# Optimization experiments

Measured on AMD Instinct MI355X. Metric: run time of the kernel, lower is better.

Reference implementation:

```python
import jax, jax.numpy as jnp
import numpy as np
import math

C = 128

def setup_inputs() -> dict:
    key = jax.random.key(0)
    ks = jax.random.split(key, 6)
    B, N, M = 4, 8192, 2048
    s = 1.0 / math.sqrt(C)
    return {
        "pcd_up": jax.random.normal(ks[0], (B, C, N), dtype=jnp.float32),
        "pcd_down": jax.random.normal(ks[1], (B, C, M), dtype=jnp.float32),
        "wq": jax.random.normal(ks[2], (C, C), dtype=jnp.float32) * s,
        "wk": jax.random.normal(ks[3], (C, C), dtype=jnp.float32) * s,
        "wv": jax.random.normal(ks[4], (C, C), dtype=jnp.float32) * s,
        "wskip": jax.random.normal(ks[5], (C, C), dtype=jnp.float32) * s,
    }

def reference(pcd_up, pcd_down, wq, wk, wv, wskip):
    # Conv1d(kernel=1, no bias) == per-point linear: w @ x over channel dim
    q = jnp.einsum('oc,bcn->bon', wq, pcd_up)      # [B,C,N]
    k = jnp.einsum('oc,bcm->bom', wk, pcd_down)    # [B,C,M]
    v = jnp.einsum('oc,bcm->bom', wv, pcd_down)    # [B,C,M]
    energy = jnp.einsum('bcn,bcm->bnm', q, k)      # [B,N,M]
    scale = math.sqrt(q.shape[1])                  # sqrt(C): q.shape[-2] in torch
    attn = jax.nn.softmax(energy / scale, axis=-1)
    x = jnp.einsum('bnm,bcm->bcn', attn, v)        # [B,C,N]
    skip = jnp.einsum('oc,bcn->bon', wskip, pcd_up)
    return skip + x
```

## Files before the change

kernel.cpp:

```cpp
#include <hip/hip_runtime.h>
#include <hip/hip_bf16.h>
#include <math.h>

#define C_DIM 128
#define B_DIM 4
#define N_DIM 8192
#define M_DIM 2048
#define NT_KV 32

typedef unsigned short u16;
typedef unsigned int u32;
typedef short bf16x8 __attribute__((ext_vector_type(8)));
typedef float f32x4 __attribute__((ext_vector_type(4)));
typedef float f32x16 __attribute__((ext_vector_type(16)));
typedef u32 u32x4 __attribute__((ext_vector_type(4)));

__device__ inline u16 f2bf(float f) {
  u32 u = __builtin_bit_cast(u32, f);
  u += 0x7fffu + ((u >> 16) & 1u);
  return (u16)(u >> 16);
}
__device__ inline u32 cvtpk_bf16(float lo, float hi) {
  u32 r;
  asm("v_cvt_pk_bf16_f32 %0, %1, %2" : "=v"(r) : "v"(lo), "v"(hi));
  return r;
}

template <int MODE>
__device__ inline void proj_pass(const float* __restrict__ W, float wscale,
                                 const u16* __restrict__ xt_s,
                                 u16* __restrict__ outh,
                                 int b, int X, int x0, int t) {
  const int l = t & 63, w = t >> 6, lr = l & 15, lh = (l >> 4) & 3;
  bf16x8 wf[2][4];
  #pragma unroll
  for (int ot = 0; ot < 2; ++ot)
    #pragma unroll
    for (int kc = 0; kc < 4; ++kc) {
      const float* wp = &W[(size_t)(w * 32 + ot * 16 + lr) * 128 + kc * 32 + lh * 8];
      float4 a0 = *(const float4*)wp;
      float4 a1 = *(const float4*)(wp + 4);
      bf16x8 f;
      f[0] = (short)f2bf(a0.x * wscale); f[1] = (short)f2bf(a0.y * wscale);
      f[2] = (short)f2bf(a0.z * wscale); f[3] = (short)f2bf(a0.w * wscale);
      f[4] = (short)f2bf(a1.x * wscale); f[5] = (short)f2bf(a1.y * wscale);
      f[6] = (short)f2bf(a1.z * wscale); f[7] = (short)f2bf(a1.w * wscale);
      wf[ot][kc] = f;
    }
  f32x4 acc[2][4];
  #pragma unroll
  for (int ot = 0; ot < 2; ++ot)
    #pragma unroll
    for (int xt = 0; xt < 4; ++xt) acc[ot][xt] = 0.f;

  #pragma unroll
  for (int xt = 0; xt < 4; ++xt) {
    int xx = xt * 16 + lr;
    #pragma unroll
    for (int kc = 0; kc < 4; ++kc) {
      bf16x8 bf = *(const bf16x8*)&xt_s[xx * 128 + ((kc * 32 + lh * 8) ^ ((xx & 15) << 3))];
      #pragma unroll
      for (int ot = 0; ot < 2; ++ot)
        acc[ot][xt] = __builtin_amdgcn_mfma_f32_16x16x32_bf16(wf[ot][kc], bf, acc[ot][xt], 0, 0, 0);
    }
  }
  #pragma unroll
  for (int ot = 0; ot < 2; ++ot) {
    int o0 = w * 32 + ot * 16 + lh * 4;
    #pragma unroll
    for (int xt = 0; xt < 4; ++xt) {
      int xg = x0 + xt * 16 + lr;
      if constexpr (MODE == 0) {
        u16 h[4];
        #pragma unroll
        for (int r = 0; r < 4; ++r) h[r] = f2bf(acc[ot][xt][r]);
        *(uint2*)&outh[((size_t)b * X + xg) * 128 + o0] = *(uint2*)h;
      } else if constexpr (MODE == 2) {
        int tt = xg >> 6, mt = (xg >> 5) & 1, ms = xg & 31;
        int kcK = o0 >> 4, lh1p = (o0 >> 3) & 1, e0 = o0 & 7;
        u16 h[4];
        #pragma unroll
        for (int r = 0; r < 4; ++r) h[r] = f2bf(acc[ot][xt][r]);
        size_t off = ((((size_t)(b * NT_KV + tt) * 2 + mt) * 8 + kcK) * 64 + (ms | (lh1p << 5))) * 8 + e0;
        *(uint2*)&outh[off] = *(uint2*)h;
      } else {
        int tt = xg >> 6, sv = (xg >> 4) & 3, lh1m = (xg >> 3) & 1, e = xg & 7;
        int ctv = o0 >> 5;
        #pragma unroll
        for (int r = 0; r < 4; ++r) {
          int cs = (o0 + r) & 31;
          size_t off = ((((size_t)(b * NT_KV + tt) * 4 + ctv) * 4 + sv) * 64 + (cs | (lh1m << 5))) * 8 + e;
          outh[off] = f2bf(acc[ot][xt][r]);
        }
      }
    }
  }
}

template <int MODE_A, int MODE_B>
__global__ __launch_bounds__(256, 2) void proj_kernel(
    const float* __restrict__ in, const float* __restrict__ WA, const float* __restrict__ WB,
    u16* __restrict__ hA, u16* __restrict__ hB, int X, float wscaleA) {
  __shared__ u16 xt_s[64 * 128];
  const int b = blockIdx.y, x0 = blockIdx.x * 64, t = threadIdx.x;
  #pragma unroll
  for (int pp = 0; pp < 8; ++pp) {
    int c = pp * 16 + (t >> 4);
    int x4 = (t & 15) * 4;
    float4 v = *(const float4*)&in[((size_t)b * 128 + c) * X + x0 + x4];
    xt_s[(x4 + 0) * 128 + (c ^ (((x4 + 0) & 15) << 3))] = f2bf(v.x);
    xt_s[(x4 + 1) * 128 + (c ^ (((x4 + 1) & 15) << 3))] = f2bf(v.y);
    xt_s[(x4 + 2) * 128 + (c ^ (((x4 + 2) & 15) << 3))] = f2bf(v.z);
    xt_s[(x4 + 3) * 128 + (c ^ (((x4 + 3) & 15) << 3))] = f2bf(v.w);
  }
  __syncthreads();
  proj_pass<MODE_A>(WA, wscaleA, xt_s, hA, b, X, x0, t);
  if constexpr (MODE_B >= 0)
    proj_pass<MODE_B>(WB, 1.0f, xt_s, hB, b, X, x0, t);
}

__device__ inline void stage_kv(const u16* __restrict__ gK, const u16* __restrict__ gV,
                                u16* lK, u16* lV, int tile, int t) {
  const u16* ks = gK + (size_t)tile * 8192;
  const u16* vs = gV + (size_t)tile * 8192;
  #pragma unroll
  for (int i = 0; i < 4; ++i) {
    int ch = t + i * 256;
    __builtin_amdgcn_global_load_lds((const __attribute__((address_space(1))) void*)(ks + ch * 8),
                                     (__attribute__((address_space(3))) void*)(lK + ch * 8), 16, 0, 0);
    __builtin_amdgcn_global_load_lds((const __attribute__((address_space(1))) void*)(vs + ch * 8),
                                     (__attribute__((address_space(3))) void*)(lV + ch * 8), 16, 0, 0);
  }
}

__global__ __launch_bounds__(256, 2) void attn_kernel(
    const u16* __restrict__ Qt, const u16* __restrict__ Kt2,
    const u16* __restrict__ Vp, const float* __restrict__ up,
    const float* __restrict__ wskip, float* __restrict__ out) {
  __shared__ u16 kv[2][2][8192];

  const int bid = blockIdx.x;
  const int xcd = bid & 7, b = xcd & 3, slot = bid >> 3;
  const int n0 = ((xcd >> 2) * 32 + slot) * 128;
  const int t = threadIdx.x, w = t >> 6, l = t & 63, lh1 = l >> 5;
  const int nq = n0 + w * 32 + (l & 31);

  bf16x8 qf[8];
  #pragma unroll
  for (int kc = 0; kc < 8; ++kc)
    qf[kc] = *(const bf16x8*)&Qt[((size_t)b * N_DIM + nq) * 128 + kc * 16 + lh1 * 8];

  const u16* gK = Kt2 + (size_t)b * 262144;
  const u16* gV = Vp + (size_t)b * 262144;

  f32x16 acco[4];
  #pragma unroll
  for (int ct = 0; ct < 4; ++ct) acco[ct] = 0.f;
  float lrun = 0.f;

  bf16x8 pf[4];
  bf16x8 vreg[16];
  #pragma unroll
  for (int s = 0; s < 4; ++s) pf[s] = (bf16x8)0;
  #pragma unroll
  for (int x = 0; x < 16; ++x) vreg[x] = (bf16x8)0;

  stage_kv(gK, gV, kv[0][0], kv[0][1], 0, t);
  __syncthreads();

  #pragma unroll 2
  for (int i = 0; i < 32; ++i) {
    const int cur = i & 1;
    if (i + 1 < 32)
      stage_kv(gK, gV, kv[cur ^ 1][0], kv[cur ^ 1][1], i + 1, t);
    const u16* kl = kv[cur][0];
    const u16* vl = kv[cur][1];

    f32x16 sacc[2];
    sacc[0] = 0.f; sacc[1] = 0.f;
    __builtin_amdgcn_s_setprio(1);
    #pragma unroll
    for (int kc = 0; kc < 8; ++kc) {
      #pragma unroll
      for (int mt = 0; mt < 2; ++mt) {
        bf16x8 kf = *(const bf16x8*)&kl[((mt * 8 + kc) * 64 + l) * 8];
        sacc[mt] = __builtin_amdgcn_mfma_f32_32x32x16_bf16(kf, qf[kc], sacc[mt], 0, 0, 0);
      }
    }
    #pragma unroll
    for (int s = 0; s < 4; ++s)
      #pragma unroll
      for (int ct = 0; ct < 4; ++ct)
        acco[ct] = __builtin_amdgcn_mfma_f32_32x32x16_bf16(vreg[ct * 4 + s], pf[s], acco[ct], 0, 0, 0);
    __builtin_amdgcn_s_setprio(0);
    __builtin_amdgcn_sched_barrier(0);

    #pragma unroll
    for (int x = 0; x < 16; ++x)
      vreg[x] = *(const bf16x8*)&vl[(x * 64 + l) * 8];

    float rs = 0.f;
    #pragma unroll
    for (int mt = 0; mt < 2; ++mt)
      #pragma unroll
      for (int r = 0; r < 16; ++r) {
        sacc[mt][r] = exp2f(sacc[mt][r]);
        rs += sacc[mt][r];
      }
    lrun += rs;
    u32 gp[8][2];
    #pragma unroll
    for (int mt = 0; mt < 2; ++mt)
      #pragma unroll
      for (int j = 0; j < 4; ++j) {
        gp[mt * 4 + j][0] = cvtpk_bf16(sacc[mt][j * 4 + 0], sacc[mt][j * 4 + 1]);
        gp[mt * 4 + j][1] = cvtpk_bf16(sacc[mt][j * 4 + 2], sacc[mt][j * 4 + 3]);
      }
    #pragma unroll
    for (int s = 0; s < 4; ++s) {
      const int ga = (s >> 1) * 4 + (s & 1) * 2, gb = ga + 1;
      u32 s0 = lh1 ? gp[ga][0] : gp[gb][0];
      u32 s1 = lh1 ? gp[ga][1] : gp[gb][1];
      u32 r0 = (u32)__shfl_xor((int)s0, 32, 64);
      u32 r1 = (u32)__shfl_xor((int)s1, 32, 64);
      u32x4 fv;
      fv.x = lh1 ? r0 : gp[ga][0];
      fv.y = lh1 ? r1 : gp[ga][1];
      fv.z = lh1 ? gp[gb][0] : r0;
      fv.w = lh1 ? gp[gb][1] : r1;
      pf[s] = __builtin_bit_cast(bf16x8, fv);
    }
    __syncthreads();
  }

  __builtin_amdgcn_s_setprio(1);
  #pragma unroll
  for (int s = 0; s < 4; ++s)
    #pragma unroll
    for (int ct = 0; ct < 4; ++ct)
      acco[ct] = __builtin_amdgcn_mfma_f32_32x32x16_bf16(vreg[ct * 4 + s], pf[s], acco[ct], 0, 0, 0);
  __builtin_amdgcn_s_setprio(0);

  float lt = lrun + __shfl_xor(lrun, 32, 64);
  float inv = 1.0f / lt;
  #pragma unroll
  for (int ct = 0; ct < 4; ++ct)
    #pragma unroll
    for (int r = 0; r < 16; ++r) acco[ct][r] *= inv;

  const float* upb = up + (size_t)b * 128 * N_DIM;
  #pragma unroll
  for (int kc = 0; kc < 8; ++kc) {
    float uv[8];
    #pragma unroll
    for (int e = 0; e < 8; ++e)
      uv[e] = upb[(size_t)(kc * 16 + lh1 * 8 + e) * N_DIM + nq];
    u32x4 ufv;
    ufv.x = cvtpk_bf16(uv[0], uv[1]);
    ufv.y = cvtpk_bf16(uv[2], uv[3]);
    ufv.z = cvtpk_bf16(uv[4], uv[5]);
    ufv.w = cvtpk_bf16(uv[6], uv[7]);
    bf16x8 upf = __builtin_bit_cast(bf16x8, ufv);
    #pragma unroll
    for (int ct = 0; ct < 4; ++ct) {
      const float* wp = &wskip[(size_t)(ct * 32 + (l & 31)) * 128 + kc * 16 + lh1 * 8];
      float4 w0 = *(const float4*)wp;
      float4 w1 = *(const float4*)(wp + 4);
      u32x4 wfv;
      wfv.x = cvtpk_bf16(w0.x, w0.y);
      wfv.y = cvtpk_bf16(w0.z, w0.w);
      wfv.z = cvtpk_bf16(w1.x, w1.y);
      wfv.w = cvtpk_bf16(w1.z, w1.w);
      bf16x8 wsf = __builtin_bit_cast(bf16x8, wfv);
      acco[ct] = __builtin_amdgcn_mfma_f32_32x32x16_bf16(wsf, upf, acco[ct], 0, 0, 0);
    }
  }

  #pragma unroll
  for (int ct = 0; ct < 4; ++ct)
    #pragma unroll
    for (int r = 0; r < 16; ++r) {
      int c = ct * 32 + (r & 3) + 8 * (r >> 2) + 4 * lh1;
      out[((size_t)b * 128 + c) * N_DIM + nq] = acco[ct][r];
    }
}

extern "C" void kernel_launch(void* const* d_in, const int* in_sizes, int n_in,
                              void* d_out, int out_size, void* d_ws, size_t ws_size,
                              hipStream_t stream) {
  const float* up    = (const float*)d_in[0];
  const float* down  = (const float*)d_in[1];
  const float* wq    = (const float*)d_in[2];
  const float* wk    = (const float*)d_in[3];
  const float* wv    = (const float*)d_in[4];
  const float* wskip = (const float*)d_in[5];
  float* out = (float*)d_out;

  u16* Qt  = (u16*)d_ws;
  u16* Kt2 = Qt + (size_t)B_DIM * N_DIM * C_DIM;
  u16* Vp  = Kt2 + (size_t)B_DIM * M_DIM * C_DIM;

  const float qscale = (float)(1.4426950408889634 / sqrt(128.0));

  hipLaunchKernelGGL((proj_kernel<0, -1>), dim3(N_DIM / 64, B_DIM), dim3(256), 0, stream,
                     up, wq, nullptr, Qt, nullptr, N_DIM, qscale);
  hipLaunchKernelGGL((proj_kernel<2, 3>), dim3(M_DIM / 64, B_DIM), dim3(256), 0, stream,
                     down, wk, wv, Kt2, Vp, M_DIM, 1.0f);
  hipLaunchKernelGGL((attn_kernel), dim3(256), dim3(256), 0, stream,
                     Qt, Kt2, Vp, up, wskip, out);
}
```

Baseline: 83.16 us.

## Split attention KV range across two blocks with atomic-flag partial merge

Each query tile's KV sweep is split into two halves processed by separate blocks, doubling the grid from 256 to 512 blocks so it better fills the GPU's compute units. Each block writes its unnormalized output and row sums to workspace, and the second block to finish (detected via an atomic counter) adds in the partner's partial and runs the skip/epilogue. This relies on the scores being computed without a running max, so partials can simply be summed. It adds a memset launch, extra global traffic for partials, and fences, and is used only when the workspace is large enough.

Result: slower. 187.3 us (+125.3%).

```diff
diff --git a/kernel.cpp b/kernel.cpp
--- a/kernel.cpp
+++ b/kernel.cpp
@@ -133,17 +133,33 @@
   }
 }
 
+template <int SPLIT>
 __global__ __launch_bounds__(256, 2) void attn_kernel(
     const u16* __restrict__ Qt, const u16* __restrict__ Kt2,
     const u16* __restrict__ Vp, const float* __restrict__ up,
-    const float* __restrict__ wskip, float* __restrict__ out) {
+    const float* __restrict__ wskip, float* __restrict__ out,
+    float* __restrict__ part, float* __restrict__ lpart,
+    unsigned* __restrict__ flags) {
   __shared__ u16 kv[2][2][8192];
+  __shared__ unsigned oldflag_s;
 
   const int bid = blockIdx.x;
   const int xcd = bid & 7, b = xcd & 3, slot = bid >> 3;
-  const int n0 = ((xcd >> 2) * 32 + slot) * 128;
+  int n0, mh, pair;
+  if constexpr (SPLIT == 2) {
+    mh = slot & 1;
+    const int ntile = (xcd >> 2) * 32 + (slot >> 1);
+    n0 = ntile * 128;
+    pair = b * 64 + ntile;
+  } else {
+    mh = 0;
+    n0 = ((xcd >> 2) * 32 + slot) * 128;
+    pair = 0;
+  }
   const int t = threadIdx.x, w = t >> 6, l = t & 63, lh1 = l >> 5;
   const int nq = n0 + w * 32 + (l & 31);
+  const int NT = NT_KV / SPLIT;
+  const int t0 = mh * NT;
 
   bf16x8 qf[8];
   #pragma unroll
@@ -165,14 +181,14 @@
   #pragma unroll
   for (int x = 0; x < 16; ++x) vreg[x] = (bf16x8)0;
 
-  stage_kv(gK, gV, kv[0][0], kv[0][1], 0, t);
+  stage_kv(gK, gV, kv[0][0], kv[0][1], t0, t);
   __syncthreads();
 
   #pragma unroll 2
-  for (int i = 0; i < 32; ++i) {
+  for (int i = 0; i < NT; ++i) {
     const int cur = i & 1;
-    if (i + 1 < 32)
-      stage_kv(gK, gV, kv[cur ^ 1][0], kv[cur ^ 1][1], i + 1, t);
+    if (i + 1 < NT)
+      stage_kv(gK, gV, kv[cur ^ 1][0], kv[cur ^ 1][1], t0 + i + 1, t);
     const u16* kl = kv[cur][0];
     const u16* vl = kv[cur][1];
 
@@ -242,6 +258,30 @@
   __builtin_amdgcn_s_setprio(0);
 
   float lt = lrun + __shfl_xor(lrun, 32, 64);
+
+  if constexpr (SPLIT == 2) {
+    float* myp = part + ((size_t)pair * 2 + mh) * 16384;
+    #pragma unroll
+    for (int ct = 0; ct < 4; ++ct)
+      #pragma unroll
+      for (int r = 0; r < 16; ++r)
+        myp[((w * 4 + ct) * 16 + r) * 64 + l] = acco[ct][r];
+    if (!lh1) lpart[((pair * 2 + mh) * 4 + w) * 32 + (l & 31)] = lt;
+    __threadfence();
+    __syncthreads();
+    if (t == 0) oldflag_s = atomicAdd(&flags[pair], 1u);
+    __syncthreads();
+    if (oldflag_s == 0) return;
+    __threadfence();
+    const float* pp = part + ((size_t)pair * 2 + (mh ^ 1)) * 16384;
+    #pragma unroll
+    for (int ct = 0; ct < 4; ++ct)
+      #pragma unroll
+      for (int r = 0; r < 16; ++r)
+        acco[ct][r] += pp[((w * 4 + ct) * 16 + r) * 64 + l];
+    lt += lpart[((pair * 2 + (mh ^ 1)) * 4 + w) * 32 + (l & 31)];
+  }
+
   float inv = 1.0f / lt;
   #pragma unroll
   for (int ct = 0; ct < 4; ++ct)
@@ -296,9 +336,18 @@
   const float* wskip = (const float*)d_in[5];
   float* out = (float*)d_out;
 
-  u16* Qt  = (u16*)d_ws;
-  u16* Kt2 = Qt + (size_t)B_DIM * N_DIM * C_DIM;
-  u16* Vp  = Kt2 + (size_t)B_DIM * M_DIM * C_DIM;
+  char* ws = (char*)d_ws;
+  u16* Qt  = (u16*)ws;
+  u16* Kt2 = (u16*)(ws + (8u << 20));
+  u16* Vp  = (u16*)(ws + (10u << 20));
+  size_t offPart  = 12u << 20;
+  size_t offLpart = offPart + (size_t)256 * 2 * 16384 * 4;
+  size_t offFlags = offLpart + (size_t)256 * 2 * 128 * 4;
+  size_t need     = offFlags + 256 * sizeof(unsigned);
+  float* part     = (float*)(ws + offPart);
+  float* lpart    = (float*)(ws + offLpart);
+  unsigned* flags = (unsigned*)(ws + offFlags);
+  const bool split = ws_size >= need;
 
   const float qscale = (float)(1.4426950408889634 / sqrt(128.0));
 
@@ -306,6 +355,12 @@
                      up, wq, nullptr, Qt, nullptr, N_DIM, qscale);
   hipLaunchKernelGGL((proj_kernel<2, 3>), dim3(M_DIM / 64, B_DIM), dim3(256), 0, stream,
                      down, wk, wv, Kt2, Vp, M_DIM, 1.0f);
-  hipLaunchKernelGGL((attn_kernel), dim3(256), dim3(256), 0, stream,
-                     Qt, Kt2, Vp, up, wskip, out);
-}
+  if (split) {
+    hipMemsetAsync(flags, 0, 256 * sizeof(unsigned), stream);
+    hipLaunchKernelGGL((attn_kernel<2>), dim3(512), dim3(256), 0, stream,
+                       Qt, Kt2, Vp, up, wskip, out, part, lpart, flags);
+  } else {
+    hipLaunchKernelGGL((attn_kernel<1>), dim3(256), dim3(256), 0, stream,
+                       Qt, Kt2, Vp, up, wskip, out, nullptr, nullptr, nullptr);
+  }
+}
```

## Split each KV tile across two wave groups and reduce partial outputs via LDS

Applied to the files above, without the earlier changes.

Doubles the attention block to 512 threads. Each pair of waves shares the same 32 queries but handles a different half of every 64-key tile, so per-wave MFMA work and register use in the loop are halved and more waves are resident on each CU. Partial output accumulators and row sums from the second wave group are written to shared memory (aliased onto the KV buffers) and summed by the first group, which then does the normalisation and the skip projection. It also replaces the shfl_xor-based P fragment shuffle with v_permlane32_swap. The cost is an extra LDS reduction step with a barrier at the end and half of the waves sitting idle during the epilogue.

Measured after the change: 74.00 us. -11.0%, faster.

```diff
diff --git a/kernel.cpp b/kernel.cpp
--- a/kernel.cpp
+++ b/kernel.cpp
@@ -124,8 +124,8 @@
   const u16* ks = gK + (size_t)tile * 8192;
   const u16* vs = gV + (size_t)tile * 8192;
   #pragma unroll
-  for (int i = 0; i < 4; ++i) {
-    int ch = t + i * 256;
+  for (int i = 0; i < 2; ++i) {
+    int ch = t + i * 512;
     __builtin_amdgcn_global_load_lds((const __attribute__((address_space(1))) void*)(ks + ch * 8),
                                      (__attribute__((address_space(3))) void*)(lK + ch * 8), 16, 0, 0);
     __builtin_amdgcn_global_load_lds((const __attribute__((address_space(1))) void*)(vs + ch * 8),
@@ -133,17 +133,22 @@
   }
 }
 
-__global__ __launch_bounds__(256, 2) void attn_kernel(
+__global__ __launch_bounds__(512, 2) void attn_kernel(
     const u16* __restrict__ Qt, const u16* __restrict__ Kt2,
     const u16* __restrict__ Vp, const float* __restrict__ up,
     const float* __restrict__ wskip, float* __restrict__ out) {
-  __shared__ u16 kv[2][2][8192];
+  __shared__ union {
+    u16 kv[2][2][8192];
+    float od[4][4096];
+  } lds;
+  __shared__ float lb[4][64];
 
   const int bid = blockIdx.x;
   const int xcd = bid & 7, b = xcd & 3, slot = bid >> 3;
   const int n0 = ((xcd >> 2) * 32 + slot) * 128;
   const int t = threadIdx.x, w = t >> 6, l = t & 63, lh1 = l >> 5;
-  const int nq = n0 + w * 32 + (l & 31);
+  const int h = w >> 2;
+  const int nq = n0 + (w & 3) * 32 + (l & 31);
 
   bf16x8 qf[8];
   #pragma unroll
@@ -158,131 +163,141 @@
   for (int ct = 0; ct < 4; ++ct) acco[ct] = 0.f;
   float lrun = 0.f;
 
-  bf16x8 pf[4];
-  bf16x8 vreg[16];
-  #pragma unroll
-  for (int s = 0; s < 4; ++s) pf[s] = (bf16x8)0;
-  #pragma unroll
-  for (int x = 0; x < 16; ++x) vreg[x] = (bf16x8)0;
-
-  stage_kv(gK, gV, kv[0][0], kv[0][1], 0, t);
+  bf16x8 pf[2];
+  bf16x8 vreg[8];
+  #pragma unroll
+  for (int u = 0; u < 2; ++u) pf[u] = (bf16x8)0;
+  #pragma unroll
+  for (int x = 0; x < 8; ++x) vreg[x] = (bf16x8)0;
+
+  stage_kv(gK, gV, lds.kv[0][0], lds.kv[0][1], 0, t);
   __syncthreads();
 
   #pragma unroll 2
-  for (int i = 0; i < 32; ++i) {
+  for (int i = 0; i < NT_KV; ++i) {
     const int cur = i & 1;
-    if (i + 1 < 32)
-      stage_kv(gK, gV, kv[cur ^ 1][0], kv[cur ^ 1][1], i + 1, t);
-    const u16* kl = kv[cur][0];
-    const u16* vl = kv[cur][1];
-
-    f32x16 sacc[2];
-    sacc[0] = 0.f; sacc[1] = 0.f;
+    if (i + 1 < NT_KV)
+      stage_kv(gK, gV, lds.kv[cur ^ 1][0], lds.kv[cur ^ 1][1], i + 1, t);
+    const u16* kl = lds.kv[cur][0];
+    const u16* vl = lds.kv[cur][1];
+
+    f32x16 sacc = 0.f;
     __builtin_amdgcn_s_setprio(1);
     #pragma unroll
     for (int kc = 0; kc < 8; ++kc) {
-      #pragma unroll
-      for (int mt = 0; mt < 2; ++mt) {
-        bf16x8 kf = *(const bf16x8*)&kl[((mt * 8 + kc) * 64 + l) * 8];
-        sacc[mt] = __builtin_amdgcn_mfma_f32_32x32x16_bf16(kf, qf[kc], sacc[mt], 0, 0, 0);
-      }
-    }
-    #pragma unroll
-    for (int s = 0; s < 4; ++s)
+      bf16x8 kf = *(const bf16x8*)&kl[((h * 8 + kc) * 64 + l) * 8];
+      sacc = __builtin_amdgcn_mfma_f32_32x32x16_bf16(kf, qf[kc], sacc, 0, 0, 0);
+    }
+    #pragma unroll
+    for (int u = 0; u < 2; ++u)
       #pragma unroll
       for (int ct = 0; ct < 4; ++ct)
-        acco[ct] = __builtin_amdgcn_mfma_f32_32x32x16_bf16(vreg[ct * 4 + s], pf[s], acco[ct], 0, 0, 0);
+        acco[ct] = __builtin_amdgcn_mfma_f32_32x32x16_bf16(vreg[ct * 2 + u], pf[u], acco[ct], 0, 0, 0);
     __builtin_amdgcn_s_setprio(0);
     __builtin_amdgcn_sched_barrier(0);
 
     #pragma unroll
-    for (int x = 0; x < 16; ++x)
-      vreg[x] = *(const bf16x8*)&vl[(x * 64 + l) * 8];
-
-    float rs = 0.f;
-    #pragma unroll
-    for (int mt = 0; mt < 2; ++mt)
+    for (int ct = 0; ct < 4; ++ct)
+      #pragma unroll
+      for (int u = 0; u < 2; ++u)
+        vreg[ct * 2 + u] = *(const bf16x8*)&vl[((ct * 4 + 2 * h + u) * 64 + l) * 8];
+
+    #pragma unroll
+    for (int r = 0; r < 16; ++r) sacc[r] = exp2f(sacc[r]);
+    {
+      float a0 = (sacc[0] + sacc[1]) + (sacc[2] + sacc[3]);
+      float a1 = (sacc[4] + sacc[5]) + (sacc[6] + sacc[7]);
+      float a2 = (sacc[8] + sacc[9]) + (sacc[10] + sacc[11]);
+      float a3 = (sacc[12] + sacc[13]) + (sacc[14] + sacc[15]);
+      lrun += (a0 + a1) + (a2 + a3);
+    }
+    u32 gp[4][2];
+    #pragma unroll
+    for (int j = 0; j < 4; ++j) {
+      gp[j][0] = cvtpk_bf16(sacc[j * 4 + 0], sacc[j * 4 + 1]);
+      gp[j][1] = cvtpk_bf16(sacc[j * 4 + 2], sacc[j * 4 + 3]);
+    }
+    #pragma unroll
+    for (int u = 0; u < 2; ++u) {
+      u32 a0 = gp[2 * u][0], a1 = gp[2 * u][1];
+      u32 b0 = gp[2 * u + 1][0], b1 = gp[2 * u + 1][1];
+      asm("v_permlane32_swap_b32 %0, %1" : "+v"(a0), "+v"(b0));
+      asm("v_permlane32_swap_b32 %0, %1" : "+v"(a1), "+v"(b1));
+      u32x4 fv; fv.x = a0; fv.y = a1; fv.z = b0; fv.w = b1;
+      pf[u] = __builtin_bit_cast(bf16x8, fv);
+    }
+    __syncthreads();
+  }
+
+  __builtin_amdgcn_s_setprio(1);
+  #pragma unroll
+  for (int u = 0; u < 2; ++u)
+    #pragma unroll
+    for (int ct = 0; ct < 4; ++ct)
+      acco[ct] = __builtin_amdgcn_mfma_f32_32x32x16_bf16(vreg[ct * 2 + u], pf[u], acco[ct], 0, 0, 0);
+  __builtin_amdgcn_s_setprio(0);
+
+  float lt = lrun + __shfl_xor(lrun, 32, 64);
+
+  if (w >= 4) {
+    float* dst = lds.od[w - 4];
+    #pragma unroll
+    for (int ct = 0; ct < 4; ++ct)
+      #pragma unroll
+      for (int r = 0; r < 16; ++r) dst[(ct * 16 + r) * 64 + l] = acco[ct][r];
+    lb[w - 4][l] = lt;
+  }
+  __syncthreads();
+  if (w < 4) {
+    const float* src = lds.od[w];
+    #pragma unroll
+    for (int ct = 0; ct < 4; ++ct)
+      #pragma unroll
+      for (int r = 0; r < 16; ++r) acco[ct][r] += src[(ct * 16 + r) * 64 + l];
+    lt += lb[w][l];
+
+    float inv = 1.0f / lt;
+    #pragma unroll
+    for (int ct = 0; ct < 4; ++ct)
+      #pragma unroll
+      for (int r = 0; r < 16; ++r) acco[ct][r] *= inv;
+
+    const float* upb = up + (size_t)b * 128 * N_DIM;
+    #pragma unroll
+    for (int kc = 0; kc < 8; ++kc) {
+      float uv[8];
+      #pragma unroll
+      for (int e = 0; e < 8; ++e)
+        uv[e] = upb[(size_t)(kc * 16 + lh1 * 8 + e) * N_DIM + nq];
+      u32x4 ufv;
+      ufv.x = cvtpk_bf16(uv[0], uv[1]);
+      ufv.y = cvtpk_bf16(uv[2], uv[3]);
+      ufv.z = cvtpk_bf16(uv[4], uv[5]);
+      ufv.w = cvtpk_bf16(uv[6], uv[7]);
+      bf16x8 upf = __builtin_bit_cast(bf16x8, ufv);
+      #pragma unroll
+      for (int ct = 0; ct < 4; ++ct) {
+        const float* wp = &wskip[(size_t)(ct * 32 + (l & 31)) * 128 + kc * 16 + lh1 * 8];
+        float4 w0 = *(const float4*)wp;
+        float4 w1 = *(const float4*)(wp + 4);
+        u32x4 wfv;
+        wfv.x = cvtpk_bf16(w0.x, w0.y);
+        wfv.y = cvtpk_bf16(w0.z, w0.w);
+        wfv.z = cvtpk_bf16(w1.x, w1.y);
+        wfv.w = cvtpk_bf16(w1.z, w1.w);
+        bf16x8 wsf = __builtin_bit_cast(bf16x8, wfv);
+        acco[ct] = __builtin_amdgcn_mfma_f32_32x32x16_bf16(wsf, upf, acco[ct], 0, 0, 0);
+      }
+    }
+
+    #pragma unroll
+    for (int ct = 0; ct < 4; ++ct)
       #pragma unroll
       for (int r = 0; r < 16; ++r) {
-        sacc[mt][r] = exp2f(sacc[mt][r]);
-        rs += sacc[mt][r];
+        int c = ct * 32 + (r & 3) + 8 * (r >> 2) + 4 * lh1;
+        out[((size_t)b * 128 + c) * N_DIM + nq] = acco[ct][r];
       }
-    lrun += rs;
-    u32 gp[8][2];
-    #pragma unroll
-    for (int mt = 0; mt < 2; ++mt)
-      #pragma unroll
-      for (int j = 0; j < 4; ++j) {
-        gp[mt * 4 + j][0] = cvtpk_bf16(sacc[mt][j * 4 + 0], sacc[mt][j * 4 + 1]);
-        gp[mt * 4 + j][1] = cvtpk_bf16(sacc[mt][j * 4 + 2], sacc[mt][j * 4 + 3]);
-      }
-    #pragma unroll
-    for (int s = 0; s < 4; ++s) {
-      const int ga = (s >> 1) * 4 + (s & 1) * 2, gb = ga + 1;
-      u32 s0 = lh1 ? gp[ga][0] : gp[gb][0];
-      u32 s1 = lh1 ? gp[ga][1] : gp[gb][1];
-      u32 r0 = (u32)__shfl_xor((int)s0, 32, 64);
-      u32 r1 = (u32)__shfl_xor((int)s1, 32, 64);
-      u32x4 fv;
-      fv.x = lh1 ? r0 : gp[ga][0];
-      fv.y = lh1 ? r1 : gp[ga][1];
-      fv.z = lh1 ? gp[gb][0] : r0;
-      fv.w = lh1 ? gp[gb][1] : r1;
-      pf[s] = __builtin_bit_cast(bf16x8, fv);
-    }
-    __syncthreads();
-  }
-
-  __builtin_amdgcn_s_setprio(1);
-  #pragma unroll
-  for (int s = 0; s < 4; ++s)
-    #pragma unroll
-    for (int ct = 0; ct < 4; ++ct)
-      acco[ct] = __builtin_amdgcn_mfma_f32_32x32x16_bf16(vreg[ct * 4 + s], pf[s], acco[ct], 0, 0, 0);
-  __builtin_amdgcn_s_setprio(0);
-
-  float lt = lrun + __shfl_xor(lrun, 32, 64);
-  float inv = 1.0f / lt;
-  #pragma unroll
-  for (int ct = 0; ct < 4; ++ct)
-    #pragma unroll
-    for (int r = 0; r < 16; ++r) acco[ct][r] *= inv;
-
-  const float* upb = up + (size_t)b * 128 * N_DIM;
-  #pragma unroll
-  for (int kc = 0; kc < 8; ++kc) {
-    float uv[8];
-    #pragma unroll
-    for (int e = 0; e < 8; ++e)
-      uv[e] = upb[(size_t)(kc * 16 + lh1 * 8 + e) * N_DIM + nq];
-    u32x4 ufv;
-    ufv.x = cvtpk_bf16(uv[0], uv[1]);
-    ufv.y = cvtpk_bf16(uv[2], uv[3]);
-    ufv.z = cvtpk_bf16(uv[4], uv[5]);
-    ufv.w = cvtpk_bf16(uv[6], uv[7]);
-    bf16x8 upf = __builtin_bit_cast(bf16x8, ufv);
-    #pragma unroll
-    for (int ct = 0; ct < 4; ++ct) {
-      const float* wp = &wskip[(size_t)(ct * 32 + (l & 31)) * 128 + kc * 16 + lh1 * 8];
-      float4 w0 = *(const float4*)wp;
-      float4 w1 = *(const float4*)(wp + 4);
-      u32x4 wfv;
-      wfv.x = cvtpk_bf16(w0.x, w0.y);
-      wfv.y = cvtpk_bf16(w0.z, w0.w);
-      wfv.z = cvtpk_bf16(w1.x, w1.y);
-      wfv.w = cvtpk_bf16(w1.z, w1.w);
-      bf16x8 wsf = __builtin_bit_cast(bf16x8, wfv);
-      acco[ct] = __builtin_amdgcn_mfma_f32_32x32x16_bf16(wsf, upf, acco[ct], 0, 0, 0);
-    }
-  }
-
-  #pragma unroll
-  for (int ct = 0; ct < 4; ++ct)
-    #pragma unroll
-    for (int r = 0; r < 16; ++r) {
-      int c = ct * 32 + (r & 3) + 8 * (r >> 2) + 4 * lh1;
-      out[((size_t)b * 128 + c) * N_DIM + nq] = acco[ct][r];
-    }
+  }
 }
 
 extern "C" void kernel_launch(void* const* d_in, const int* in_sizes, int n_in,
@@ -306,6 +321,6 @@
                      up, wq, nullptr, Qt, nullptr, N_DIM, qscale);
   hipLaunchKernelGGL((proj_kernel<2, 3>), dim3(M_DIM / 64, B_DIM), dim3(256), 0, stream,
                      down, wk, wv, Kt2, Vp, M_DIM, 1.0f);
-  hipLaunchKernelGGL((attn_kernel), dim3(256), dim3(256), 0, stream,
+  hipLaunchKernelGGL((attn_kernel), dim3(256), dim3(512), 0, stream,
                      Qt, Kt2, Vp, up, wskip, out);
 }
```
